# Kernel tuning notes

Hardware: AMD Instinct MI355X
Metric: run time of the kernel (lower is better)

The kernel has to match this reference:

```python
import jax, jax.numpy as jnp
import numpy as np

N_NODES = 100000
N_EDGES = 1600000
IN_CH, HID, OUT_CH = 512, 32, 64


def setup_inputs() -> dict:
    key = jax.random.key(0)
    ks = jax.random.split(key, 8)
    x = jax.random.normal(ks[0], (N_NODES, IN_CH), dtype=jnp.float32)
    edge_index = jax.random.randint(ks[1], (2, N_EDGES), 0, N_NODES, dtype=jnp.int64)
    def glorot(k, fan_in, fan_out):
        lim = np.sqrt(6.0 / (fan_in + fan_out)).astype(np.float32)
        return jax.random.uniform(k, (fan_in, fan_out), jnp.float32, -lim, lim)
    return {
        "x": x,
        "edge_index": edge_index,
        "W1": glorot(ks[2], IN_CH, HID), "b1": jnp.zeros((HID,), jnp.float32),
        "W2": glorot(ks[3], HID, HID),   "b2": jnp.zeros((HID,), jnp.float32),
        "W3": glorot(ks[4], HID, OUT_CH),"b3": jnp.zeros((OUT_CH,), jnp.float32),
    }


def _gcn_norm(edge_index, n_nodes):
    # PyG GCNConv: add self-loops, symmetric normalization D^-1/2 (A+I) D^-1/2
    loops = jnp.arange(n_nodes, dtype=edge_index.dtype)
    src = jnp.concatenate([edge_index[0], loops])
    dst = jnp.concatenate([edge_index[1], loops])
    deg = jax.ops.segment_sum(jnp.ones_like(dst, dtype=jnp.float32), dst,
                              num_segments=n_nodes)
    dinv = jnp.where(deg > 0, jax.lax.rsqrt(deg), 0.0)
    norm = dinv[src] * dinv[dst]  # [E + N]
    return src, dst, norm


def _gcn_conv(x, W, b, src, dst, norm, n_nodes):
    h = x @ W                                  # [N, F_out] dense GEMM
    msg = h[src] * norm[:, None]               # gather + scale over edges
    out = jax.ops.segment_sum(msg, dst, num_segments=n_nodes)  # scatter-add
    return out + b


def reference(x, edge_index, W1, b1, W2, b2, W3, b3):
    n = x.shape[0]
    src, dst, norm = _gcn_norm(edge_index, n)
    h = _gcn_conv(x, W1, b1, src, dst, norm, n)
    h = jax.nn.relu(h)  # dropout is identity in eval mode (training=False)
    h = _gcn_conv(h, W2, b2, src, dst, norm, n)
    h = jax.nn.relu(h)
    h = _gcn_conv(h, W3, b3, src, dst, norm, n)
    return jax.nn.log_softmax(h, axis=1)
```

## Files before the change

kernel.cpp:

```cpp
#include <hip/hip_runtime.h>
#include <math.h>

static constexpr int NN    = 100000;
static constexpr int NBUCK = (NN + 255) / 256;
static constexpr int NBLK_A = 256;

#define CDIV(a,b) (((a)+(b)-1)/(b))

typedef __attribute__((ext_vector_type(8))) short bf16x8;
typedef __attribute__((ext_vector_type(4))) float f32x4;

__device__ __forceinline__ float bf2f(unsigned short u) {
    return __uint_as_float(((unsigned)u) << 16);
}
__device__ __forceinline__ unsigned short f2bf(float f) {
    unsigned u = __float_as_uint(f);
    u += 0x7fffu + ((u >> 16) & 1u);
    return (unsigned short)(u >> 16);
}

__global__ __launch_bounds__(256) void k_count(const int* __restrict__ dst,
                                               const float* __restrict__ W1,
                                               int* __restrict__ gcnt,
                                               unsigned short* __restrict__ WT,
                                               int E, int chunk) {
    const int b = blockIdx.x;
    const int t = threadIdx.x;
    if (b >= NBLK_A) {
        int base = (b - NBLK_A) * 8192 + t;
        #pragma unroll
        for (int i = 0; i < 32; i++) {
            int idx = base + i * 256;
            int k = idx >> 5, c = idx & 31;
            WT[c * 512 + (((k >> 3) ^ (c & 7)) << 3) + (k & 7)] = f2bf(W1[idx]);
        }
        return;
    }
    __shared__ int lc[NBUCK];
    for (int i = t; i < NBUCK; i += 256) lc[i] = 0;
    __syncthreads();
    int e0 = b * chunk;
    int e1 = e0 + chunk; if (e1 > E) e1 = E;
    for (int e = e0 + t; e < e1; e += 256)
        atomicAdd(&lc[dst[e] >> 8], 1);
    __syncthreads();
    for (int i = t; i < NBUCK; i += 256)
        gcnt[i * NBLK_A + b] = lc[i];
}

__global__ __launch_bounds__(256) void k_scan2(const int* __restrict__ gcnt,
                                               int* __restrict__ gofs,
                                               int* __restrict__ bcnt) {
    const int b = blockIdx.x, t = threadIdx.x;
    __shared__ int sm[256];
    int v = gcnt[b * NBLK_A + t];
    sm[t] = v; __syncthreads();
    for (int off = 1; off < 256; off <<= 1) {
        int u = (t >= off) ? sm[t - off] : 0;
        __syncthreads();
        sm[t] += u;
        __syncthreads();
    }
    gofs[b * NBLK_A + t] = sm[t] - v;
    if (t == 255) bcnt[b] = sm[255];
}

__global__ __launch_bounds__(512) void k_scanB(const int* __restrict__ bcnt,
                                               int* __restrict__ bbase, int E) {
    __shared__ int sm[512];
    int t = threadIdx.x;
    int v = (t < NBUCK) ? bcnt[t] : 0;
    sm[t] = v; __syncthreads();
    for (int off = 1; off < 512; off <<= 1) {
        int u = (t >= off) ? sm[t - off] : 0;
        __syncthreads();
        sm[t] += u;
        __syncthreads();
    }
    if (t < NBUCK) bbase[t] = sm[t] - v;
    if (t == 0) bbase[NBUCK] = E;
}

__global__ __launch_bounds__(256) void k_bpart(const int* __restrict__ src,
                                               const int* __restrict__ dst,
                                               const int* __restrict__ bbase,
                                               const int* __restrict__ gofs,
                                               unsigned int* __restrict__ part,
                                               int E, int chunk) {
    __shared__ int boff[NBUCK];
    __shared__ int lc[NBUCK];
    const int blk = blockIdx.x;
    for (int i = threadIdx.x; i < NBUCK; i += 256) {
        boff[i] = bbase[i] + gofs[i * NBLK_A + blk];
        lc[i] = 0;
    }
    __syncthreads();
    int e0 = blk * chunk;
    int e1 = e0 + chunk; if (e1 > E) e1 = E;
    for (int e = e0 + threadIdx.x; e < e1; e += 256) {
        int d = dst[e];
        int b = d >> 8;
        int pos = boff[b] + atomicAdd(&lc[b], 1);
        part[pos] = ((unsigned)src[e] << 8) | (unsigned)(d & 255);
    }
}

__global__ __launch_bounds__(256) void k_bbuild(const unsigned int* __restrict__ part,
                                                const int* __restrict__ bbase,
                                                int* __restrict__ row_ptr,
                                                float* __restrict__ dinv,
                                                int* __restrict__ col, int n, int E) {
    __shared__ int hist[256];
    __shared__ int excl[256];
    __shared__ int fill[256];
    const int b = blockIdx.x;
    const int t = threadIdx.x;
    const int e0 = bbase[b], e1 = bbase[b + 1];
    hist[t] = 0; fill[t] = 0;
    __syncthreads();
    for (int e = e0 + t; e < e1; e += 256)
        atomicAdd(&hist[part[e] & 255], 1);
    __syncthreads();
    int v = hist[t];
    excl[t] = v; __syncthreads();
    for (int off = 1; off < 256; off <<= 1) {
        int u = (t >= off) ? excl[t - off] : 0;
        __syncthreads();
        excl[t] += u;
        __syncthreads();
    }
    int ex = excl[t] - v;
    int g = b * 256 + t;
    if (g < n) {
        row_ptr[g] = e0 + ex;
        dinv[g] = rsqrtf((float)(v + 1));
    }
    if (b == 0 && t == 0) row_ptr[n] = E;
    excl[t] = e0 + ex;
    __syncthreads();
    for (int e = e0 + t; e < e1; e += 256) {
        unsigned u = part[e];
        int ld = u & 255;
        int pos = excl[ld] + atomicAdd(&fill[ld], 1);
        col[pos] = (int)(u >> 8);
    }
}

__global__ __launch_bounds__(256) void k_gemm1(const float* __restrict__ X,
                                               const unsigned short* __restrict__ WT,
                                               const float* __restrict__ dinv,
                                               unsigned short* __restrict__ OUT,
                                               int nrows) {
    __shared__ unsigned short wt[32][512];
    const int t = threadIdx.x;
    {
        const uint4* s = (const uint4*)WT;
        uint4* d = (uint4*)&wt[0][0];
        #pragma unroll
        for (int i = 0; i < 8; i++) d[t + 256 * i] = s[t + 256 * i];
    }
    __syncthreads();

    const int lane  = t & 63;
    const int w     = t >> 6;
    const int grow0 = blockIdx.x * 64 + w * 16;
    const int m     = lane & 15;
    const int kb    = lane >> 4;
    int row = grow0 + m; if (row > nrows - 1) row = nrows - 1;
    const float* xrow = X + (size_t)row * 512 + kb * 8;

    f32x4 acc0 = {0.f, 0.f, 0.f, 0.f};
    f32x4 acc1 = {0.f, 0.f, 0.f, 0.f};
    const int mx  = m & 7;
    const unsigned short* wrow0 = &wt[m][0];
    const unsigned short* wrow1 = &wt[m + 16][0];

    #pragma unroll 4
    for (int kk = 0; kk < 512; kk += 32) {
        float4 xa = *(const float4*)(xrow + kk);
        float4 xb = *(const float4*)(xrow + kk + 4);
        bf16x8 a;
        a[0] = (short)f2bf(xa.x); a[1] = (short)f2bf(xa.y);
        a[2] = (short)f2bf(xa.z); a[3] = (short)f2bf(xa.w);
        a[4] = (short)f2bf(xb.x); a[5] = (short)f2bf(xb.y);
        a[6] = (short)f2bf(xb.z); a[7] = (short)f2bf(xb.w);
        const int g = (kk >> 3) + kb;
        bf16x8 b0 = *(const bf16x8*)&wrow0[((g ^ mx) & 63) * 8];
        bf16x8 b1 = *(const bf16x8*)&wrow1[((g ^ mx) & 63) * 8];
        acc0 = __builtin_amdgcn_mfma_f32_16x16x32_bf16(a, b0, acc0, 0, 0, 0);
        acc1 = __builtin_amdgcn_mfma_f32_16x16x32_bf16(a, b1, acc1, 0, 0, 0);
    }
    #pragma unroll
    for (int j = 0; j < 4; j++) {
        int rr = grow0 + kb * 4 + j;
        if (rr < nrows) {
            float d = dinv[rr];
            OUT[(size_t)rr * 32 + m]      = f2bf(acc0[j] * d);
            OUT[(size_t)rr * 32 + 16 + m] = f2bf(acc1[j] * d);
        }
    }
}

__device__ __forceinline__ float4 agg_gather_bf16(const unsigned short* __restrict__ HS,
                                                  const int* __restrict__ col,
                                                  int s0, int s1, int node, int c0) {
    float4 a0 = {0,0,0,0}, a1 = {0,0,0,0}, a2 = {0,0,0,0}, a3 = {0,0,0,0};
    int e = s0;
    for (; e + 3 < s1; e += 4) {
        int sA = col[e], sB = col[e + 1], sC = col[e + 2], sD = col[e + 3];
        ushort4 uA = *(const ushort4*)&HS[(size_t)sA * 32 + c0];
        ushort4 uB = *(const ushort4*)&HS[(size_t)sB * 32 + c0];
        ushort4 uC = *(const ushort4*)&HS[(size_t)sC * 32 + c0];
        ushort4 uD = *(const ushort4*)&HS[(size_t)sD * 32 + c0];
        a0.x += bf2f(uA.x); a0.y += bf2f(uA.y); a0.z += bf2f(uA.z); a0.w += bf2f(uA.w);
        a1.x += bf2f(uB.x); a1.y += bf2f(uB.y); a1.z += bf2f(uB.z); a1.w += bf2f(uB.w);
        a2.x += bf2f(uC.x); a2.y += bf2f(uC.y); a2.z += bf2f(uC.z); a2.w += bf2f(uC.w);
        a3.x += bf2f(uD.x); a3.y += bf2f(uD.y); a3.z += bf2f(uD.z); a3.w += bf2f(uD.w);
    }
    for (; e < s1; e++) {
        int sA = col[e];
        ushort4 uA = *(const ushort4*)&HS[(size_t)sA * 32 + c0];
        a0.x += bf2f(uA.x); a0.y += bf2f(uA.y); a0.z += bf2f(uA.z); a0.w += bf2f(uA.w);
    }
    ushort4 uS = *(const ushort4*)&HS[(size_t)node * 32 + c0];
    float4 acc;
    acc.x = a0.x + a1.x + a2.x + a3.x + bf2f(uS.x);
    acc.y = a0.y + a1.y + a2.y + a3.y + bf2f(uS.y);
    acc.z = a0.z + a1.z + a2.z + a3.z + bf2f(uS.z);
    acc.w = a0.w + a1.w + a2.w + a3.w + bf2f(uS.w);
    return acc;
}

__global__ __launch_bounds__(256) void k_fuse32(const unsigned short* __restrict__ HS,
                                                const int* __restrict__ row_ptr,
                                                const int* __restrict__ col,
                                                const float* __restrict__ dinv,
                                                const float* __restrict__ bin,
                                                const float* __restrict__ W,
                                                unsigned short* __restrict__ OUT, int n) {
    __shared__ float ws[32][32];
    {
        int i = threadIdx.x;
        int r = i / 8, c = (i % 8) * 4;
        *(float4*)&ws[r][c] = *(const float4*)&W[r * 32 + c];
    }
    __syncthreads();
    const int t    = threadIdx.x;
    const int node = blockIdx.x * 32 + t / 8;
    const int c0   = (t % 8) * 4;
    if (node >= n) return;
    const int s0 = row_ptr[node], s1 = row_ptr[node + 1];
    float4 acc = agg_gather_bf16(HS, col, s0, s1, node, c0);
    const float di = dinv[node];
    float4 b4 = *(const float4*)&bin[c0];
    float4 a;
    a.x = fmaxf(di * acc.x + b4.x, 0.f);
    a.y = fmaxf(di * acc.y + b4.y, 0.f);
    a.z = fmaxf(di * acc.z + b4.z, 0.f);
    a.w = fmaxf(di * acc.w + b4.w, 0.f);
    float4 o = {0,0,0,0};
    const int gb = (t & 63) & ~7;
    #pragma unroll
    for (int s = 0; s < 8; s++) {
        float4 as;
        as.x = __shfl(a.x, gb + s, 64);
        as.y = __shfl(a.y, gb + s, 64);
        as.z = __shfl(a.z, gb + s, 64);
        as.w = __shfl(a.w, gb + s, 64);
        const int k0 = s * 4;
        float4 w0 = *(const float4*)&ws[k0 + 0][c0];
        float4 w1 = *(const float4*)&ws[k0 + 1][c0];
        float4 w2 = *(const float4*)&ws[k0 + 2][c0];
        float4 w3 = *(const float4*)&ws[k0 + 3][c0];
        o.x += as.x*w0.x + as.y*w1.x + as.z*w2.x + as.w*w3.x;
        o.y += as.x*w0.y + as.y*w1.y + as.z*w2.y + as.w*w3.y;
        o.z += as.x*w0.z + as.y*w1.z + as.z*w2.z + as.w*w3.z;
        o.w += as.x*w0.w + as.y*w1.w + as.z*w2.w + as.w*w3.w;
    }
    ushort4 st;
    st.x = f2bf(o.x * di); st.y = f2bf(o.y * di);
    st.z = f2bf(o.z * di); st.w = f2bf(o.w * di);
    *(ushort4*)&OUT[(size_t)node * 32 + c0] = st;
}

__global__ __launch_bounds__(256) void k_aggscale(const unsigned short* __restrict__ HS,
                                                  const int* __restrict__ row_ptr,
                                                  const int* __restrict__ col,
                                                  const float* __restrict__ dinv,
                                                  const float* __restrict__ bin,
                                                  unsigned short* __restrict__ OUT, int n) {
    const int t    = threadIdx.x;
    const int node = blockIdx.x * 32 + t / 8;
    const int c0   = (t % 8) * 4;
    if (node >= n) return;
    const int s0 = row_ptr[node], s1 = row_ptr[node + 1];
    float4 acc = agg_gather_bf16(HS, col, s0, s1, node, c0);
    const float di = dinv[node];
    float4 b4 = *(const float4*)&bin[c0];
    ushort4 o;
    o.x = f2bf(di * fmaxf(di * acc.x + b4.x, 0.f));
    o.y = f2bf(di * fmaxf(di * acc.y + b4.y, 0.f));
    o.z = f2bf(di * fmaxf(di * acc.z + b4.z, 0.f));
    o.w = f2bf(di * fmaxf(di * acc.w + b4.w, 0.f));
    *(ushort4*)&OUT[(size_t)node * 32 + c0] = o;
}

__global__ __launch_bounds__(256) void k_fuseC(const unsigned short* __restrict__ YS,
                                               const int* __restrict__ row_ptr,
                                               const int* __restrict__ col,
                                               const float* __restrict__ dinv,
                                               const float* __restrict__ b3,
                                               const float* __restrict__ W,
                                               float* __restrict__ OUT, int n) {
    __shared__ float ws[32][64];
    {
        int i = threadIdx.x;
        int r0w = i / 16, cw = (i % 16) * 4;
        *(float4*)&ws[r0w][cw]      = *(const float4*)&W[r0w * 64 + cw];
        *(float4*)&ws[r0w + 16][cw] = *(const float4*)&W[(r0w + 16) * 64 + cw];
    }
    __syncthreads();
    const int t    = threadIdx.x;
    const int node = blockIdx.x * 32 + t / 8;
    const int c0   = (t % 8) * 4;
    if (node >= n) return;
    const int s0 = row_ptr[node], s1 = row_ptr[node + 1];
    float4 acc = agg_gather_bf16(YS, col, s0, s1, node, c0);
    const float di = dinv[node];
    float4 g;
    g.x = di * acc.x; g.y = di * acc.y; g.z = di * acc.z; g.w = di * acc.w;
    float4 oL = {0,0,0,0}, oH = {0,0,0,0};
    const int gb = (t & 63) & ~7;
    #pragma unroll
    for (int s = 0; s < 8; s++) {
        float4 gs;
        gs.x = __shfl(g.x, gb + s, 64);
        gs.y = __shfl(g.y, gb + s, 64);
        gs.z = __shfl(g.z, gb + s, 64);
        gs.w = __shfl(g.w, gb + s, 64);
        const int k0 = s * 4;
        #pragma unroll
        for (int q = 0; q < 4; q++) {
            float gv = (q == 0) ? gs.x : (q == 1) ? gs.y : (q == 2) ? gs.z : gs.w;
            float4 wL = *(const float4*)&ws[k0 + q][c0];
            float4 wH = *(const float4*)&ws[k0 + q][32 + c0];
            oL.x += gv * wL.x; oL.y += gv * wL.y; oL.z += gv * wL.z; oL.w += gv * wL.w;
            oH.x += gv * wH.x; oH.y += gv * wH.y; oH.z += gv * wH.z; oH.w += gv * wH.w;
        }
    }
    float4 bL = *(const float4*)&b3[c0];
    float4 bH = *(const float4*)&b3[32 + c0];
    oL.x += bL.x; oL.y += bL.y; oL.z += bL.z; oL.w += bL.w;
    oH.x += bH.x; oH.y += bH.y; oH.z += bH.z; oH.w += bH.w;
    float m = fmaxf(fmaxf(fmaxf(oL.x, oL.y), fmaxf(oL.z, oL.w)),
                    fmaxf(fmaxf(oH.x, oH.y), fmaxf(oH.z, oH.w)));
    #pragma unroll
    for (int off = 1; off < 8; off <<= 1) m = fmaxf(m, __shfl_xor(m, off, 64));
    float sum = expf(oL.x - m) + expf(oL.y - m) + expf(oL.z - m) + expf(oL.w - m)
              + expf(oH.x - m) + expf(oH.y - m) + expf(oH.z - m) + expf(oH.w - m);
    #pragma unroll
    for (int off = 1; off < 8; off <<= 1) sum += __shfl_xor(sum, off, 64);
    float lse = m + logf(sum);
    float4 rL, rH;
    rL.x = oL.x - lse; rL.y = oL.y - lse; rL.z = oL.z - lse; rL.w = oL.w - lse;
    rH.x = oH.x - lse; rH.y = oH.y - lse; rH.z = oH.z - lse; rH.w = oH.w - lse;
    *(float4*)&OUT[(size_t)node * 64 + c0]      = rL;
    *(float4*)&OUT[(size_t)node * 64 + 32 + c0] = rH;
}

extern "C" void kernel_launch(void* const* d_in, const int* in_sizes, int n_in,
                              void* d_out, int out_size, void* d_ws, size_t ws_size,
                              hipStream_t stream) {
    const float* x  = (const float*)d_in[0];
    const int*   ei = (const int*)d_in[1];
    const float* W1 = (const float*)d_in[2];
    const float* b1 = (const float*)d_in[3];
    const float* W2 = (const float*)d_in[4];
    const float* b2 = (const float*)d_in[5];
    const float* W3 = (const float*)d_in[6];
    const float* b3 = (const float*)d_in[7];
    float* out = (float*)d_out;

    const int E = in_sizes[1] / 2;
    const int n = NN;
    const int* src = ei;
    const int* dst = ei + E;

    char* p = (char*)d_ws;
    auto alloc = [&](size_t bytes) -> void* {
        void* r = p;
        p += (bytes + 63) & ~(size_t)63;
        return r;
    };
    int*            gcnt    = (int*)alloc((size_t)NBUCK * NBLK_A * 4);
    int*            gofs    = (int*)alloc((size_t)NBUCK * NBLK_A * 4);
    int*            bcnt    = (int*)alloc((size_t)NBUCK * 4);
    int*            bbase   = (int*)alloc((size_t)(NBUCK + 1) * 4);
    unsigned*       part    = (unsigned*)alloc((size_t)E * 4);
    int*            row_ptr = (int*)alloc((size_t)(n + 1) * 4);
    int*            col     = (int*)alloc((size_t)E * 4);
    float*          dinv    = (float*)alloc((size_t)n * 4);
    unsigned short* wtbf    = (unsigned short*)alloc((size_t)512 * 32 * 2);
    unsigned short* hs1     = (unsigned short*)alloc((size_t)n * 32 * 2);
    unsigned short* hs2     = (unsigned short*)alloc((size_t)n * 32 * 2);

    const int chunk = CDIV(E, NBLK_A);

    k_count<<<NBLK_A + 2, 256, 0, stream>>>(dst, W1, gcnt, wtbf, E, chunk);
    k_scan2<<<NBUCK, 256, 0, stream>>>(gcnt, gofs, bcnt);
    k_scanB<<<1, 512, 0, stream>>>(bcnt, bbase, E);
    k_bpart<<<NBLK_A, 256, 0, stream>>>(src, dst, bbase, gofs, part, E, chunk);
    k_bbuild<<<NBUCK, 256, 0, stream>>>(part, bbase, row_ptr, dinv, col, n, E);

    k_gemm1<<<CDIV(n, 64), 256, 0, stream>>>(x, wtbf, dinv, hs1, n);
    k_fuse32<<<CDIV(n, 32), 256, 0, stream>>>(hs1, row_ptr, col, dinv, b1, W2, hs2, n);
    k_aggscale<<<CDIV(n, 32), 256, 0, stream>>>(hs2, row_ptr, col, dinv, b2, hs1, n);
    k_fuseC<<<CDIV(n, 32), 256, 0, stream>>>(hs1, row_ptr, col, dinv, b3, W3, out, n);
}
```

Before: 181.0 us.

## Sort nodes by degree and process aggregation kernels in degree order

Builds a degree histogram during CSR construction, scans it, and computes a permutation of nodes ordered by in-degree (counting sort). The three aggregation kernels then process nodes through this permutation so that the 8-lane groups within a wavefront handle nodes of similar degree, cutting divergence from uneven neighbor-loop lengths. The cost is two extra small kernels, an extra indirection load per node, and loss of spatial locality in the row_ptr, dinv and output accesses. With random graphs the degree variance is modest, so the balance gain may be small.

```diff
diff --git a/kernel.cpp b/kernel.cpp
--- a/kernel.cpp
+++ b/kernel.cpp
@@ -23,9 +23,14 @@
                                                const float* __restrict__ W1,
                                                int* __restrict__ gcnt,
                                                unsigned short* __restrict__ WT,
+                                               int* __restrict__ dhist,
                                                int E, int chunk) {
     const int b = blockIdx.x;
     const int t = threadIdx.x;
+    if (b == NBLK_A + 2) {
+        dhist[t] = 0; dhist[t + 256] = 0;
+        return;
+    }
     if (b >= NBLK_A) {
         int base = (b - NBLK_A) * 8192 + t;
         #pragma unroll
@@ -109,14 +114,17 @@
                                                 const int* __restrict__ bbase,
                                                 int* __restrict__ row_ptr,
                                                 float* __restrict__ dinv,
+                                                int* __restrict__ deg,
+                                                int* __restrict__ dhist,
                                                 int* __restrict__ col, int n, int E) {
     __shared__ int hist[256];
     __shared__ int excl[256];
     __shared__ int fill[256];
+    __shared__ int dh[512];
     const int b = blockIdx.x;
     const int t = threadIdx.x;
     const int e0 = bbase[b], e1 = bbase[b + 1];
-    hist[t] = 0; fill[t] = 0;
+    hist[t] = 0; fill[t] = 0; dh[t] = 0; dh[t + 256] = 0;
     __syncthreads();
     for (int e = e0 + t; e < e1; e += 256)
         atomicAdd(&hist[part[e] & 255], 1);
@@ -134,6 +142,9 @@
     if (g < n) {
         row_ptr[g] = e0 + ex;
         dinv[g] = rsqrtf((float)(v + 1));
+        deg[g] = v;
+        int bin = v < 511 ? v : 511;
+        atomicAdd(&dh[bin], 1);
     }
     if (b == 0 && t == 0) row_ptr[n] = E;
     excl[t] = e0 + ex;
@@ -143,6 +154,51 @@
         int ld = u & 255;
         int pos = excl[ld] + atomicAdd(&fill[ld], 1);
         col[pos] = (int)(u >> 8);
+    }
+    for (int i = t; i < 512; i += 256)
+        if (dh[i]) atomicAdd(&dhist[i], dh[i]);
+}
+
+__global__ __launch_bounds__(512) void k_dscan(const int* __restrict__ dhist,
+                                               int* __restrict__ dfill) {
+    __shared__ int sm[512];
+    int t = threadIdx.x;
+    int v = dhist[t];
+    sm[t] = v; __syncthreads();
+    for (int off = 1; off < 512; off <<= 1) {
+        int u = (t >= off) ? sm[t - off] : 0;
+        __syncthreads();
+        sm[t] += u;
+        __syncthreads();
+    }
+    dfill[t] = sm[t] - v;
+}
+
+__global__ __launch_bounds__(256) void k_dperm(const int* __restrict__ deg,
+                                               int* __restrict__ dfill,
+                                               int* __restrict__ perm, int n) {
+    __shared__ int lc[512];
+    __shared__ int lb[512];
+    const int t = threadIdx.x;
+    lc[t] = 0; lc[t + 256] = 0;
+    __syncthreads();
+    int i = blockIdx.x * 256 + t;
+    int bin = -1;
+    if (i < n) {
+        int v = deg[i];
+        bin = v < 511 ? v : 511;
+        atomicAdd(&lc[bin], 1);
+    }
+    __syncthreads();
+    for (int j = t; j < 512; j += 256) {
+        int c = lc[j];
+        lb[j] = c ? atomicAdd(&dfill[j], c) : 0;
+        lc[j] = 0;
+    }
+    __syncthreads();
+    if (i < n) {
+        int pos = lb[bin] + atomicAdd(&lc[bin], 1);
+        perm[pos] = i;
     }
 }
 
@@ -234,6 +290,7 @@
 __global__ __launch_bounds__(256) void k_fuse32(const unsigned short* __restrict__ HS,
                                                 const int* __restrict__ row_ptr,
                                                 const int* __restrict__ col,
+                                                const int* __restrict__ perm,
                                                 const float* __restrict__ dinv,
                                                 const float* __restrict__ bin,
                                                 const float* __restrict__ W,
@@ -245,10 +302,11 @@
         *(float4*)&ws[r][c] = *(const float4*)&W[r * 32 + c];
     }
     __syncthreads();
-    const int t    = threadIdx.x;
-    const int node = blockIdx.x * 32 + t / 8;
-    const int c0   = (t % 8) * 4;
-    if (node >= n) return;
+    const int t   = threadIdx.x;
+    const int idx = blockIdx.x * 32 + t / 8;
+    const int c0  = (t % 8) * 4;
+    if (idx >= n) return;
+    const int node = perm[idx];
     const int s0 = row_ptr[node], s1 = row_ptr[node + 1];
     float4 acc = agg_gather_bf16(HS, col, s0, s1, node, c0);
     const float di = dinv[node];
@@ -286,13 +344,15 @@
 __global__ __launch_bounds__(256) void k_aggscale(const unsigned short* __restrict__ HS,
                                                   const int* __restrict__ row_ptr,
                                                   const int* __restrict__ col,
+                                                  const int* __restrict__ perm,
                                                   const float* __restrict__ dinv,
                                                   const float* __restrict__ bin,
                                                   unsigned short* __restrict__ OUT, int n) {
-    const int t    = threadIdx.x;
-    const int node = blockIdx.x * 32 + t / 8;
-    const int c0   = (t % 8) * 4;
-    if (node >= n) return;
+    const int t   = threadIdx.x;
+    const int idx = blockIdx.x * 32 + t / 8;
+    const int c0  = (t % 8) * 4;
+    if (idx >= n) return;
+    const int node = perm[idx];
     const int s0 = row_ptr[node], s1 = row_ptr[node + 1];
     float4 acc = agg_gather_bf16(HS, col, s0, s1, node, c0);
     const float di = dinv[node];
@@ -308,6 +368,7 @@
 __global__ __launch_bounds__(256) void k_fuseC(const unsigned short* __restrict__ YS,
                                                const int* __restrict__ row_ptr,
                                                const int* __restrict__ col,
+                                               const int* __restrict__ perm,
                                                const float* __restrict__ dinv,
                                                const float* __restrict__ b3,
                                                const float* __restrict__ W,
@@ -320,10 +381,11 @@
         *(float4*)&ws[r0w + 16][cw] = *(const float4*)&W[(r0w + 16) * 64 + cw];
     }
     __syncthreads();
-    const int t    = threadIdx.x;
-    const int node = blockIdx.x * 32 + t / 8;
-    const int c0   = (t % 8) * 4;
-    if (node >= n) return;
+    const int t   = threadIdx.x;
+    const int idx = blockIdx.x * 32 + t / 8;
+    const int c0  = (t % 8) * 4;
+    if (idx >= n) return;
+    const int node = perm[idx];
     const int s0 = row_ptr[node], s1 = row_ptr[node + 1];
     float4 acc = agg_gather_bf16(YS, col, s0, s1, node, c0);
     const float di = dinv[node];
@@ -400,20 +462,26 @@
     int*            row_ptr = (int*)alloc((size_t)(n + 1) * 4);
     int*            col     = (int*)alloc((size_t)E * 4);
     float*          dinv    = (float*)alloc((size_t)n * 4);
+    int*            deg     = (int*)alloc((size_t)n * 4);
+    int*            dhist   = (int*)alloc(512 * 4);
+    int*            dfill   = (int*)alloc(512 * 4);
+    int*            perm    = (int*)alloc((size_t)n * 4);
     unsigned short* wtbf    = (unsigned short*)alloc((size_t)512 * 32 * 2);
     unsigned short* hs1     = (unsigned short*)alloc((size_t)n * 32 * 2);
     unsigned short* hs2     = (unsigned short*)alloc((size_t)n * 32 * 2);
 
     const int chunk = CDIV(E, NBLK_A);
 
-    k_count<<<NBLK_A + 2, 256, 0, stream>>>(dst, W1, gcnt, wtbf, E, chunk);
+    k_count<<<NBLK_A + 3, 256, 0, stream>>>(dst, W1, gcnt, wtbf, dhist, E, chunk);
     k_scan2<<<NBUCK, 256, 0, stream>>>(gcnt, gofs, bcnt);
     k_scanB<<<1, 512, 0, stream>>>(bcnt, bbase, E);
     k_bpart<<<NBLK_A, 256, 0, stream>>>(src, dst, bbase, gofs, part, E, chunk);
-    k_bbuild<<<NBUCK, 256, 0, stream>>>(part, bbase, row_ptr, dinv, col, n, E);
+    k_bbuild<<<NBUCK, 256, 0, stream>>>(part, bbase, row_ptr, dinv, deg, dhist, col, n, E);
+    k_dscan<<<1, 512, 0, stream>>>(dhist, dfill);
+    k_dperm<<<CDIV(n, 256), 256, 0, stream>>>(deg, dfill, perm, n);
 
     k_gemm1<<<CDIV(n, 64), 256, 0, stream>>>(x, wtbf, dinv, hs1, n);
-    k_fuse32<<<CDIV(n, 32), 256, 0, stream>>>(hs1, row_ptr, col, dinv, b1, W2, hs2, n);
-    k_aggscale<<<CDIV(n, 32), 256, 0, stream>>>(hs2, row_ptr, col, dinv, b2, hs1, n);
-    k_fuseC<<<CDIV(n, 32), 256, 0, stream>>>(hs1, row_ptr, col, dinv, b3, W3, out, n);
-}
+    k_fuse32<<<CDIV(n, 32), 256, 0, stream>>>(hs1, row_ptr, col, perm, dinv, b1, W2, hs2, n);
+    k_aggscale<<<CDIV(n, 32), 256, 0, stream>>>(hs2, row_ptr, col, perm, dinv, b2, hs1, n);
+    k_fuseC<<<CDIV(n, 32), 256, 0, stream>>>(hs1, row_ptr, col, perm, dinv, b3, W3, out, n);
+}
```

After: 196.3 us. 1.08x slower.
